# Kernel optimization log

Measured on AMD Instinct MI355X. Metric: run time of the kernel, lower is better.

Reference implementation:

```python
import jax, jax.numpy as jnp
import numpy as np

B, N, D_OBJ, D_Q, D_FUSED, D_BOX, D_ATT = 64, 36, 2048, 2048, 2048, 4, 512


def setup_inputs() -> dict:
    key = jax.random.key(0)
    ks = jax.random.split(key, 12)
    s = lambda d: 1.0 / np.sqrt(d)
    return {
        "question_embedding": jax.random.normal(ks[0], (B * N, D_Q), jnp.float32),
        "object_features_list": jax.random.normal(ks[1], (B, N, D_OBJ), jnp.float32),
        "bounding_boxes": jax.random.uniform(ks[2], (B, N, D_BOX), jnp.float32),
        "Wq": jax.random.normal(ks[3], (D_Q, D_FUSED), jnp.float32) * s(D_Q),
        "Wo": jax.random.normal(ks[4], (D_OBJ, D_FUSED), jnp.float32) * s(D_OBJ),
        "Wfa": jax.random.normal(ks[5], (D_FUSED, D_FUSED), jnp.float32) * s(D_FUSED),
        "Wfb": jax.random.normal(ks[6], (D_FUSED, D_FUSED), jnp.float32) * s(D_FUSED),
        "Wba": jax.random.normal(ks[7], (D_BOX, D_FUSED), jnp.float32) * s(D_BOX),
        "Wbb": jax.random.normal(ks[8], (D_BOX, D_FUSED), jnp.float32) * s(D_BOX),
        "W0": jax.random.normal(ks[9], (D_FUSED, D_ATT), jnp.float32) * s(D_FUSED),
        "b0": jnp.zeros((D_ATT,), jnp.float32),
        "W1": jax.random.normal(ks[10], (D_ATT, 1), jnp.float32) * s(D_ATT),
        "b1": jnp.zeros((1,), jnp.float32),
        "batch_size": B,
        "num_obj": N,
    }


def reference(question_embedding, object_features_list, bounding_boxes,
              Wq, Wo, Wfa, Wfb, Wba, Wbb, W0, b0, W1, b1,
              batch_size, num_obj):
    # fuse_object_features_with_questions: MLB fusion of question and objects
    obj_flat = object_features_list.reshape(batch_size * num_obj, -1)  # [BN, D]
    fused = (question_embedding @ Wq) * (obj_flat @ Wo)                # [BN, Df]
    fused = fused.reshape(batch_size, num_obj, -1)                     # [B, N, Df]

    # pairwise: project once, broadcast-multiply instead of materializing
    # expanded [B*N*N, D] operands (same math as expand+view+fusion).
    ra = fused @ Wfa                 # [B, N, Df]
    rb = fused @ Wfb                 # [B, N, Df]
    ba = bounding_boxes @ Wba        # [B, N, Df]
    bb = bounding_boxes @ Wbb        # [B, N, Df]
    # relations[b, i, j, :] = fusion_fused(f_i, f_j) + fusion_box(box_i, box_j)
    relations = ra[:, :, None, :] * rb[:, None, :, :] + ba[:, :, None, :] * bb[:, None, :, :]  # [B,N,N,Df]

    # compute_relation_attention: linear-tanh-linear, softmax over dim=2
    h = jnp.tanh(relations @ W0 + b0)          # [B, N, N, D_att]
    scores = h @ W1 + b1                       # [B, N, N, 1]
    att = jax.nn.softmax(scores, axis=2)[..., 0]  # [B, N, N]
    e_hat = jnp.sum(relations * att[..., None], axis=2)  # [B, N, Df]

    pairwise_res = fused + e_hat
    return object_features_list + pairwise_res
```

## Files before the change

kernel.cpp:

```cpp
#include <hip/hip_runtime.h>
#include <hip/hip_bf16.h>
#include <math.h>

constexpr int kB    = 64;
constexpr int kN    = 36;
constexpr int kBN   = kB * kN;
constexpr int kD    = 2048;
constexpr int kDatt = 512;
constexpr int kPairs = kN * kN;

using bf16x8 = __attribute__((ext_vector_type(8))) short;
using f32x4  = __attribute__((ext_vector_type(4))) float;

typedef unsigned int u32;
typedef __attribute__((address_space(3))) u32 lds_u32;
typedef const __attribute__((address_space(1))) u32 glb_u32;

__device__ inline unsigned short f2bf(float f) {
    union { float f; unsigned u; } v; v.f = f;
    unsigned r = v.u + 0x7FFFu + ((v.u >> 16) & 1u);
    return (unsigned short)(r >> 16);
}

__global__ __launch_bounds__(256)
void kcvt(const float* __restrict__ x, unsigned short* __restrict__ y, int n4)
{
    int i = blockIdx.x * 256 + threadIdx.x;
    if (i < n4) {
        float4 v = ((const float4*)x)[i];
        ushort4 o = {f2bf(v.x), f2bf(v.y), f2bf(v.z), f2bf(v.w)};
        ((ushort4*)y)[i] = o;
    }
}

__global__ __launch_bounds__(256)
void ktrp(const float* __restrict__ W, unsigned short* __restrict__ WT, int nt)
{
    __shared__ float T[64][65];
    const int k0 = blockIdx.x * 64;
    const int n0 = blockIdx.y * 64;
    const int c = threadIdx.x & 63, r0 = threadIdx.x >> 6;
    #pragma unroll
    for (int rr = 0; rr < 64; rr += 4)
        T[r0 + rr][c] = W[(size_t)(k0 + r0 + rr) * nt + n0 + c];
    __syncthreads();
    #pragma unroll
    for (int rr = 0; rr < 64; rr += 4)
        WT[(size_t)(n0 + r0 + rr) * kD + k0 + c] = f2bf(T[c][r0 + rr]);
}

__global__ __launch_bounds__(64)
void krepack_w0(const unsigned short* __restrict__ W0T, unsigned short* __restrict__ W0s)
{
    const int kb    = blockIdx.x;
    const int chunk = blockIdx.y;
    const int g     = threadIdx.x;
    const int row = chunk * 16 + (g & 7) + ((g >> 5) << 3);
    const int cg8 = ((g >> 3) & 3) * 8;
    const uint4 v = *(const uint4*)&W0T[(size_t)row * kD + kb * 32 + cg8];
    *(uint4*)&W0s[(size_t)kb * 16384 + chunk * 512 + g * 8] = v;
}

__global__ __launch_bounds__(256)
void kgbox(const float* __restrict__ Wba, const float* __restrict__ Wbb,
           const float* __restrict__ W0, float* __restrict__ Gpart)
{
    __shared__ float red[4][64][17];
    const int ct = blockIdx.x;
    const int kc = blockIdx.y;
    const int cl = threadIdx.x & 63;
    const int kq = threadIdx.x >> 6;
    const int c  = ct * 64 + cl;

    float acc[16];
    #pragma unroll
    for (int t = 0; t < 16; ++t) acc[t] = 0.f;

    const int kbase = kc * 128 + kq * 32;
    for (int kk = 0; kk < 32; ++kk) {
        int k = kbase + kk;
        float w0 = W0[(size_t)k * kDatt + c];
        float a0 = Wba[k], a1 = Wba[kD + k], a2 = Wba[2 * kD + k], a3 = Wba[3 * kD + k];
        float b0 = Wbb[k] * w0, b1 = Wbb[kD + k] * w0,
              b2 = Wbb[2 * kD + k] * w0, b3 = Wbb[3 * kD + k] * w0;
        acc[0]  = fmaf(a0, b0, acc[0]);  acc[1]  = fmaf(a0, b1, acc[1]);
        acc[2]  = fmaf(a0, b2, acc[2]);  acc[3]  = fmaf(a0, b3, acc[3]);
        acc[4]  = fmaf(a1, b0, acc[4]);  acc[5]  = fmaf(a1, b1, acc[5]);
        acc[6]  = fmaf(a1, b2, acc[6]);  acc[7]  = fmaf(a1, b3, acc[7]);
        acc[8]  = fmaf(a2, b0, acc[8]);  acc[9]  = fmaf(a2, b1, acc[9]);
        acc[10] = fmaf(a2, b2, acc[10]); acc[11] = fmaf(a2, b3, acc[11]);
        acc[12] = fmaf(a3, b0, acc[12]); acc[13] = fmaf(a3, b1, acc[13]);
        acc[14] = fmaf(a3, b2, acc[14]); acc[15] = fmaf(a3, b3, acc[15]);
    }
    #pragma unroll
    for (int t = 0; t < 16; ++t) red[kq][cl][t] = acc[t];
    __syncthreads();
    #pragma unroll
    for (int t = 0; t < 4; ++t) {
        int s = threadIdx.x + t * 256;
        int cc = s >> 4, uv = s & 15;
        float v = red[0][cc][uv] + red[1][cc][uv] + red[2][cc][uv] + red[3][cc][uv];
        Gpart[((size_t)kc * 16 + uv) * kDatt + ct * 64 + cc] = v;
    }
}

__global__ __launch_bounds__(64)
void krepack_g(const float* __restrict__ Gpart, unsigned short* __restrict__ W0s)
{
    const int chunk = blockIdx.x;
    const int g     = threadIdx.x;
    const int col = chunk * 16 + (g & 7) + ((g >> 5) << 3);
    const int kg  = (g >> 3) & 3;
    unsigned short o[8];
    #pragma unroll
    for (int e = 0; e < 8; ++e) {
        int kl = kg * 8 + e;
        if (kl < 16) {
            float s = 0.f;
            #pragma unroll
            for (int kc = 0; kc < 16; ++kc)
                s += Gpart[((size_t)kc * 16 + kl) * kDatt + col];
            o[e] = f2bf(s);
        } else o[e] = 0;
    }
    *(uint4*)&W0s[(size_t)64 * 16384 + chunk * 512 + g * 8] = *(uint4*)o;
}

__device__ inline void stage128(const unsigned short* __restrict__ g,
                                int grow0, int k0,
                                unsigned short* lds, int w, int lane)
{
    const int sr = lane >> 2, sc = (lane & 3) * 8;
    #pragma unroll
    for (int t = 0; t < 2; ++t) {
        int r = w * 32 + t * 16;
        const unsigned short* gp = g + (size_t)(grow0 + r + sr) * kD + k0 + sc;
        __builtin_amdgcn_global_load_lds((glb_u32*)gp, (lds_u32*)(lds + r * 32), 16, 0, 0);
    }
}
__device__ inline void stage64(const unsigned short* __restrict__ g,
                               int grow0, int k0,
                               unsigned short* lds, int w, int lane)
{
    const int sr = lane >> 2, sc = (lane & 3) * 8;
    int r = w * 16;
    const unsigned short* gp = g + (size_t)(grow0 + r + sr) * kD + k0 + sc;
    __builtin_amdgcn_global_load_lds((glb_u32*)gp, (lds_u32*)(lds + r * 32), 16, 0, 0);
}

__global__ __launch_bounds__(256, 2)
void k1_dual_mfma(const unsigned short* __restrict__ Qb,
                  const unsigned short* __restrict__ WqT,
                  const unsigned short* __restrict__ Ob,
                  const unsigned short* __restrict__ WoT,
                  unsigned short* __restrict__ fusedb)
{
    __shared__ __align__(16) unsigned short As1[128][32];
    __shared__ __align__(16) unsigned short As2[128][32];
    __shared__ __align__(16) unsigned short Bs1[64][32];
    __shared__ __align__(16) unsigned short Bs2[64][32];

    const int tid = threadIdx.x;
    const int lane = tid & 63;
    const int w = tid >> 6;
    const int wm = w >> 1, wn = w & 1;
    const int row0 = blockIdx.y * 128;
    const int col0 = blockIdx.x * 64;

    f32x4 acc1[4][2], acc2[4][2];
    #pragma unroll
    for (int mt = 0; mt < 4; ++mt)
        #pragma unroll
        for (int nt = 0; nt < 2; ++nt) { acc1[mt][nt] = (f32x4)(0.f); acc2[mt][nt] = (f32x4)(0.f); }

    const int fr = lane & 15, ko = (lane >> 4) * 8;

    for (int k0 = 0; k0 < kD; k0 += 32) {
        stage128(Qb,  row0, k0, &As1[0][0], w, lane);
        stage128(Ob,  row0, k0, &As2[0][0], w, lane);
        stage64 (WqT, col0, k0, &Bs1[0][0], w, lane);
        stage64 (WoT, col0, k0, &Bs2[0][0], w, lane);
        __syncthreads();

        bf16x8 a1[4], a2[4];
        #pragma unroll
        for (int mt = 0; mt < 4; ++mt) {
            a1[mt] = *(bf16x8*)&As1[wm * 64 + mt * 16 + fr][ko];
            a2[mt] = *(bf16x8*)&As2[wm * 64 + mt * 16 + fr][ko];
        }
        #pragma unroll
        for (int nt = 0; nt < 2; ++nt) {
            bf16x8 b1 = *(bf16x8*)&Bs1[wn * 32 + nt * 16 + fr][ko];
            bf16x8 b2 = *(bf16x8*)&Bs2[wn * 32 + nt * 16 + fr][ko];
            #pragma unroll
            for (int mt = 0; mt < 4; ++mt) {
                acc1[mt][nt] = __builtin_amdgcn_mfma_f32_16x16x32_bf16(a1[mt], b1, acc1[mt][nt], 0, 0, 0);
                acc2[mt][nt] = __builtin_amdgcn_mfma_f32_16x16x32_bf16(a2[mt], b2, acc2[mt][nt], 0, 0, 0);
            }
        }
        __syncthreads();
    }

    const int fq = lane >> 4;
    #pragma unroll
    for (int mt = 0; mt < 4; ++mt)
        #pragma unroll
        for (int nt = 0; nt < 2; ++nt) {
            int row = row0 + wm * 64 + mt * 16 + fq * 4;
            int col = col0 + wn * 32 + nt * 16 + fr;
            #pragma unroll
            for (int reg = 0; reg < 4; ++reg) {
                float v = acc1[mt][nt][reg] * acc2[mt][nt][reg];
                fusedb[(size_t)(row + reg) * kD + col] = f2bf(v);
            }
        }
}

__global__ __launch_bounds__(256, 2)
void k2_dual_mfma(const unsigned short* __restrict__ Fb,
                  const unsigned short* __restrict__ WfaT,
                  const unsigned short* __restrict__ WfbT,
                  float* __restrict__ ra, float* __restrict__ rb)
{
    __shared__ __align__(16) unsigned short As [128][32];
    __shared__ __align__(16) unsigned short Bs1[64][32];
    __shared__ __align__(16) unsigned short Bs2[64][32];

    const int tid = threadIdx.x;
    const int lane = tid & 63;
    const int w = tid >> 6;
    const int wm = w >> 1, wn = w & 1;
    const int row0 = blockIdx.y * 128;
    const int col0 = blockIdx.x * 64;

    f32x4 acc1[4][2], acc2[4][2];
    #pragma unroll
    for (int mt = 0; mt < 4; ++mt)
        #pragma unroll
        for (int nt = 0; nt < 2; ++nt) { acc1[mt][nt] = (f32x4)(0.f); acc2[mt][nt] = (f32x4)(0.f); }

    const int fr = lane & 15, ko = (lane >> 4) * 8;

    for (int k0 = 0; k0 < kD; k0 += 32) {
        stage128(Fb,   row0, k0, &As [0][0], w, lane);
        stage64 (WfaT, col0, k0, &Bs1[0][0], w, lane);
        stage64 (WfbT, col0, k0, &Bs2[0][0], w, lane);
        __syncthreads();

        bf16x8 a[4];
        #pragma unroll
        for (int mt = 0; mt < 4; ++mt)
            a[mt] = *(bf16x8*)&As[wm * 64 + mt * 16 + fr][ko];
        #pragma unroll
        for (int nt = 0; nt < 2; ++nt) {
            bf16x8 b1 = *(bf16x8*)&Bs1[wn * 32 + nt * 16 + fr][ko];
            bf16x8 b2 = *(bf16x8*)&Bs2[wn * 32 + nt * 16 + fr][ko];
            #pragma unroll
            for (int mt = 0; mt < 4; ++mt) {
                acc1[mt][nt] = __builtin_amdgcn_mfma_f32_16x16x32_bf16(a[mt], b1, acc1[mt][nt], 0, 0, 0);
                acc2[mt][nt] = __builtin_amdgcn_mfma_f32_16x16x32_bf16(a[mt], b2, acc2[mt][nt], 0, 0, 0);
            }
        }
        __syncthreads();
    }

    const int fq = lane >> 4;
    #pragma unroll
    for (int mt = 0; mt < 4; ++mt)
        #pragma unroll
        for (int nt = 0; nt < 2; ++nt) {
            int row = row0 + wm * 64 + mt * 16 + fq * 4;
            int col = col0 + wn * 32 + nt * 16 + fr;
            #pragma unroll
            for (int reg = 0; reg < 4; ++reg) {
                size_t o = (size_t)(row + reg) * kD + col;
                ra[o] = acc1[mt][nt][reg];
                rb[o] = acc2[mt][nt][reg];
            }
        }
}

__global__ __launch_bounds__(1024)
void k4_scores_mfma(const float* __restrict__ ra, const float* __restrict__ rb,
                    const float* __restrict__ box,
                    const unsigned short* __restrict__ W0s,
                    const float* __restrict__ b0, const float* __restrict__ W1,
                    float* __restrict__ scores)
{
    __shared__ __align__(16) unsigned short Bs[2][512 * 32];
    __shared__ __align__(16) unsigned short RelS[2][128][40];
    __shared__ __align__(16) float4 Stg4[2][378];
    __shared__ float scoreS[128];

    const int tid  = threadIdx.x;
    const int lane = tid & 63;
    const int w    = tid >> 6;
    const int wm   = w >> 3;
    const int wn   = w & 7;

    const int work = (blockIdx.x & 7) * 88 + (blockIdx.x >> 3);
    const int b    = work / 11;
    const int tile = work - b * 11;
    const int p0   = tile * 128;
    const int i0   = p0 / kN;

    const float* raB  = ra  + (size_t)b * kN * kD;
    const float* rbB  = rb  + (size_t)b * kN * kD;
    const float* boxB = box + (size_t)b * kN * 4;

    const bool hasStage = (tid < 336);
    const float* sptr;
    int sdst;
    {
        int s = hasStage ? tid : 335;
        int row = s >> 3, q = s & 7;
        int grow; const float* base;
        if (row < 6) {
            int il = (row < 5) ? row : 4;
            grow = i0 + il; if (grow > kN - 1) grow = kN - 1;
            base = raB;
        } else {
            grow = row - 6;
            base = rbB;
        }
        sptr = base + (size_t)grow * kD + q * 4;
        sdst = row * 9 + q;
    }

    int rowA, cgA, ilA, iA, jA;
    {
        rowA = tid >> 3; cgA = tid & 7;
        int p = p0 + rowA; if (p >= kPairs) p = kPairs - 1;
        iA  = p / kN;
        jA  = p - iA * kN;
        ilA = iA - i0;
    }

    const int fr = lane & 15, fq = lane >> 4;
    const int bco = ((fr & 7) << 3) + ((fr >> 3) << 8) + (fq << 6);

    f32x4 acc[4][4];
    #pragma unroll
    for (int mt = 0; mt < 4; ++mt)
        #pragma unroll
        for (int nt = 0; nt < 4; ++nt)
            acc[mt][nt] = (f32x4)(0.f);

    if (tid < 128) scoreS[tid] = 0.f;

    float4 sreg0;

    #define ISSUE_B(k0_, buf_)                                                   \
        _Pragma("unroll")                                                        \
        for (int t = 0; t < 2; ++t) {                                            \
            int chunk = w * 2 + t;                                               \
            const unsigned short* gp = W0s + (size_t)((k0_) >> 5) * 16384        \
                                       + chunk * 512 + lane * 8;                 \
            __builtin_amdgcn_global_load_lds((glb_u32*)gp,                       \
                (lds_u32*)&Bs[buf_][chunk * 512], 16, 0, 0);                     \
        }

    #define STAGE_LOAD(k0_) {                                                    \
            if (hasStage) sreg0 = *(const float4*)(sptr + (k0_));                \
        }

    #define STAGE_WRITE(buf_) {                                                  \
            if (hasStage) Stg4[buf_][sdst] = sreg0;                              \
        }

    #define REL_GEN(buf_) {                                                      \
            float4 va = Stg4[buf_][ilA * 9 + cgA];                               \
            float4 vr = Stg4[buf_][(6 + jA) * 9 + cgA];                          \
            ushort4 o;                                                           \
            o.x = f2bf(va.x * vr.x);                                             \
            o.y = f2bf(va.y * vr.y);                                             \
            o.z = f2bf(va.z * vr.z);                                             \
            o.w = f2bf(va.w * vr.w);                                             \
            *(ushort4*)&RelS[buf_][rowA][cgA * 4] = o;                           \
        }

    #define REL_GEN_BOX(buf_) {                                                  \
            ushort4 o = {0, 0, 0, 0};                                            \
            if (cgA < 4) {                                                       \
                float4 bi = *(const float4*)(boxB + iA * 4);                     \
                float4 bj = *(const float4*)(boxB + jA * 4);                     \
                float biu = (cgA == 0) ? bi.x : (cgA == 1) ? bi.y                \
                          : (cgA == 2) ? bi.z : bi.w;                            \
                o.x = f2bf(biu * bj.x);                                          \
                o.y = f2bf(biu * bj.y);                                          \
                o.z = f2bf(biu * bj.z);                                          \
                o.w = f2bf(biu * bj.w);                                          \
            }                                                                    \
            *(ushort4*)&RelS[buf_][rowA][cgA * 4] = o;                           \
        }

    STAGE_LOAD(0)
    STAGE_WRITE(0)
    STAGE_LOAD(32)
    __syncthreads();
    REL_GEN(0)
    STAGE_WRITE(1)
    ISSUE_B(0, 0)

    for (int k = 0; k <= 64; ++k) {
        const int cur = k & 1, nxt = cur ^ 1;
        __syncthreads();
        if (k < 62) STAGE_LOAD((k + 2) * 32)
        if (k < 64) ISSUE_B((k + 1) * 32, nxt)
        bf16x8 af[4];
        #pragma unroll
        for (int mt = 0; mt < 4; ++mt)
            af[mt] = *(bf16x8*)&RelS[cur][wm * 64 + mt * 16 + fr][fq * 8];
        if (k < 63) REL_GEN(nxt)
        else if (k == 63) REL_GEN_BOX(nxt)
        __builtin_amdgcn_s_setprio(1);
        #pragma unroll
        for (int nt = 0; nt < 4; ++nt) {
            bf16x8 bfv = *(bf16x8*)&Bs[cur][wn * 2048 + nt * 512 + bco];
            #pragma unroll
            for (int mt = 0; mt < 4; ++mt)
                acc[mt][nt] = __builtin_amdgcn_mfma_f32_16x16x32_bf16(af[mt], bfv, acc[mt][nt], 0, 0, 0);
        }
        __builtin_amdgcn_s_setprio(0);
        if (k < 62) STAGE_WRITE(cur)
    }

    float b0v[4], w1v[4];
    #pragma unroll
    for (int nt = 0; nt < 4; ++nt) {
        int col = wn * 64 + nt * 16 + fr;
        b0v[nt] = b0[col];
        w1v[nt] = W1[col];
    }
    #pragma unroll
    for (int mt = 0; mt < 4; ++mt) {
        #pragma unroll
        for (int reg = 0; reg < 4; ++reg) {
            float p = 0.f;
            #pragma unroll
            for (int nt = 0; nt < 4; ++nt)
                p += w1v[nt] * tanhf(acc[mt][nt][reg] + b0v[nt]);
            p += __shfl_xor(p, 1, 64);
            p += __shfl_xor(p, 2, 64);
            p += __shfl_xor(p, 4, 64);
            p += __shfl_xor(p, 8, 64);
            if (fr == 0)
                atomicAdd(&scoreS[wm * 64 + mt * 16 + fq * 4 + reg], p);
        }
    }
    __syncthreads();
    if (tid < 128 && p0 + tid < kPairs)
        scores[(size_t)b * kPairs + p0 + tid] = scoreS[tid];
}

__global__ __launch_bounds__(64)
void k5_softmax(const float* __restrict__ scores, const float* __restrict__ box,
                float* __restrict__ att, float* __restrict__ abox)
{
    const int bi = blockIdx.x;
    const int b  = bi / kN;
    const int tid = threadIdx.x;
    float s = (tid < kN) ? scores[(size_t)bi * kN + tid] : -1e30f;
    float m = s;
    #pragma unroll
    for (int off = 32; off >= 1; off >>= 1)
        m = fmaxf(m, __shfl_xor(m, off, 64));
    float e = (tid < kN) ? expf(s - m) : 0.f;
    float sum = e;
    #pragma unroll
    for (int off = 32; off >= 1; off >>= 1)
        sum += __shfl_xor(sum, off, 64);
    float a = e / sum;
    if (tid < kN) att[(size_t)bi * kN + tid] = a;

    float4 bx = {0.f, 0.f, 0.f, 0.f};
    if (tid < kN) bx = *(const float4*)(box + (size_t)(b * kN + tid) * 4);
    bx.x *= a; bx.y *= a; bx.z *= a; bx.w *= a;
    #pragma unroll
    for (int off = 32; off >= 1; off >>= 1) {
        bx.x += __shfl_xor(bx.x, off, 64);
        bx.y += __shfl_xor(bx.y, off, 64);
        bx.z += __shfl_xor(bx.z, off, 64);
        bx.w += __shfl_xor(bx.w, off, 64);
    }
    if (tid == 0) *(float4*)(abox + (size_t)bi * 4) = bx;
}

__global__ __launch_bounds__(256)
void k6_output(const float* __restrict__ obj, const unsigned short* __restrict__ fusedb,
               const float* __restrict__ ra, const float* __restrict__ rb,
               const float* __restrict__ att, const float* __restrict__ box,
               const float* __restrict__ abox,
               const float* __restrict__ Wba, const float* __restrict__ Wbb,
               float* __restrict__ out)
{
    __shared__ float attS[kN];
    const int bi = blockIdx.x;
    const int b = bi / kN;
    const int tid = threadIdx.x;
    if (tid < kN) attS[tid] = att[(size_t)bi * kN + tid];
    __syncthreads();
    const float4 bxi = *(const float4*)(box  + (size_t)bi * 4);
    const float4 axi = *(const float4*)(abox + (size_t)bi * 4);
    for (int d = tid; d < kD; d += 256) {
        float s1 = 0.f;
        #pragma unroll 4
        for (int j = 0; j < kN; ++j)
            s1 = fmaf(attS[j], rb[(size_t)(b * kN + j) * kD + d], s1);
        float bav = bxi.x * Wba[d] + bxi.y * Wba[kD + d]
                  + bxi.z * Wba[2 * kD + d] + bxi.w * Wba[3 * kD + d];
        float s2  = axi.x * Wbb[d] + axi.y * Wbb[kD + d]
                  + axi.z * Wbb[2 * kD + d] + axi.w * Wbb[3 * kD + d];
        size_t o = (size_t)bi * kD + d;
        float fv = __uint_as_float((u32)fusedb[o] << 16);
        out[o] = obj[o] + fv + ra[o] * s1 + bav * s2;
    }
}

extern "C" void kernel_launch(void* const* d_in, const int* in_sizes, int n_in,
                              void* d_out, int out_size, void* d_ws, size_t ws_size,
                              hipStream_t stream)
{
    const float* q   = (const float*)d_in[0];
    const float* obj = (const float*)d_in[1];
    const float* box = (const float*)d_in[2];
    const float* Wq  = (const float*)d_in[3];
    const float* Wo  = (const float*)d_in[4];
    const float* Wfa = (const float*)d_in[5];
    const float* Wfb = (const float*)d_in[6];
    const float* Wba = (const float*)d_in[7];
    const float* Wbb = (const float*)d_in[8];
    const float* W0  = (const float*)d_in[9];
    const float* b0v = (const float*)d_in[10];
    const float* W1  = (const float*)d_in[11];
    float* out = (float*)d_out;

    const size_t nBD = (size_t)kBN * kD;
    float* ws = (float*)d_ws;
    size_t off = 0;
    float* ra     = ws + off; off += nBD;
    float* rb     = ws + off; off += nBD;
    float* scores = ws + off; off += (size_t)kBN * kN;
    float* att    = ws + off; off += (size_t)kBN * kN;
    float* abox   = ws + off; off += (size_t)kBN * 4;
    float* Gpart  = ws + off; off += (size_t)16 * 16 * kDatt;

    unsigned short* us = (unsigned short*)(ws + off);
    size_t uoff = 0;
    unsigned short* W0T     = us + uoff; uoff += (size_t)kDatt * kD;
    unsigned short* W0s     = us + uoff; uoff += (size_t)65 * 16384;
    unsigned short* q_bf    = us + uoff; uoff += nBD;
    unsigned short* obj_bf  = us + uoff; uoff += nBD;
    unsigned short* fusedbf = us + uoff; uoff += nBD;
    unsigned short* WqT     = us + uoff; uoff += (size_t)kD * kD;
    unsigned short* WoT     = us + uoff; uoff += (size_t)kD * kD;
    unsigned short* WfaT = q_bf;
    unsigned short* WfbT = obj_bf;

    const int n4 = (int)(nBD / 4);
    kcvt<<<dim3((n4 + 255) / 256), 256, 0, stream>>>(q,   q_bf,   n4);
    kcvt<<<dim3((n4 + 255) / 256), 256, 0, stream>>>(obj, obj_bf, n4);
    ktrp<<<dim3(32, 32), 256, 0, stream>>>(Wq, WqT, kD);
    ktrp<<<dim3(32, 32), 256, 0, stream>>>(Wo, WoT, kD);
    ktrp<<<dim3(32, 8),  256, 0, stream>>>(W0, W0T, kDatt);
    krepack_w0<<<dim3(kD / 32, kDatt / 16), 64, 0, stream>>>(W0T, W0s);
    kgbox<<<dim3(8, 16), 256, 0, stream>>>(Wba, Wbb, W0, Gpart);
    krepack_g<<<dim3(32), 64, 0, stream>>>(Gpart, W0s);

    k1_dual_mfma<<<dim3(kD / 64, kBN / 128), 256, 0, stream>>>(q_bf, WqT, obj_bf, WoT, fusedbf);

    ktrp<<<dim3(32, 32), 256, 0, stream>>>(Wfa, WfaT, kD);
    ktrp<<<dim3(32, 32), 256, 0, stream>>>(Wfb, WfbT, kD);

    k2_dual_mfma<<<dim3(kD / 64, kBN / 128), 256, 0, stream>>>(fusedbf, WfaT, WfbT, ra, rb);

    k4_scores_mfma<<<dim3(kB * 11), 1024, 0, stream>>>(ra, rb, box, W0s, b0v, W1, scores);
    k5_softmax<<<kBN, 64, 0, stream>>>(scores, box, att, abox);
    k6_output<<<kBN, 256, 0, stream>>>(obj, fusedbf, ra, rb, att, box, abox, Wba, Wbb, out);
}
```

Measured before the change: 658.3 us.

## Split score kernel across two attention-column halves with atomic accumulation

The relation-attention score kernel now splits the 512 attention columns into two halves handled by separate 512-thread blocks, doubling the grid. Each block accumulates its partial score into a pre-zeroed scores buffer with global atomics, and a zeroing kernel is added before launch. The smaller blocks and halved B-tile shared memory are meant to improve occupancy and scheduling. In exchange, the relation products and staging loads are computed redundantly in both halves, and atomics make the summation order nondeterministic.

```diff
diff --git a/kernel.cpp b/kernel.cpp
--- a/kernel.cpp
+++ b/kernel.cpp
@@ -31,6 +31,13 @@
         ushort4 o = {f2bf(v.x), f2bf(v.y), f2bf(v.z), f2bf(v.w)};
         ((ushort4*)y)[i] = o;
     }
+}
+
+__global__ __launch_bounds__(256)
+void kzero(float* __restrict__ p, int n)
+{
+    int i = blockIdx.x * 256 + threadIdx.x;
+    if (i < n) p[i] = 0.f;
 }
 
 __global__ __launch_bounds__(256)
@@ -280,14 +287,14 @@
         }
 }
 
-__global__ __launch_bounds__(1024)
+__global__ __launch_bounds__(512, 4)
 void k4_scores_mfma(const float* __restrict__ ra, const float* __restrict__ rb,
                     const float* __restrict__ box,
                     const unsigned short* __restrict__ W0s,
                     const float* __restrict__ b0, const float* __restrict__ W1,
                     float* __restrict__ scores)
 {
-    __shared__ __align__(16) unsigned short Bs[2][512 * 32];
+    __shared__ __align__(16) unsigned short Bs[2][256 * 32];
     __shared__ __align__(16) unsigned short RelS[2][128][40];
     __shared__ __align__(16) float4 Stg4[2][378];
     __shared__ float scoreS[128];
@@ -295,12 +302,14 @@
     const int tid  = threadIdx.x;
     const int lane = tid & 63;
     const int w    = tid >> 6;
-    const int wm   = w >> 3;
-    const int wn   = w & 7;
-
-    const int work = (blockIdx.x & 7) * 88 + (blockIdx.x >> 3);
-    const int b    = work / 11;
-    const int tile = work - b * 11;
+    const int wm   = w >> 2;
+    const int wn   = w & 3;
+
+    const int work = (blockIdx.x & 7) * 176 + (blockIdx.x >> 3);
+    const int colb = work & 1;
+    const int wt   = work >> 1;
+    const int b    = wt / 11;
+    const int tile = wt - b * 11;
     const int p0   = tile * 128;
     const int i0   = p0 / kN;
 
@@ -327,13 +336,15 @@
         sdst = row * 9 + q;
     }
 
-    int rowA, cgA, ilA, iA, jA;
+    int rowA, cg2, iA, jA, sA, sR;
     {
-        rowA = tid >> 3; cgA = tid & 7;
+        rowA = tid >> 2; cg2 = tid & 3;
         int p = p0 + rowA; if (p >= kPairs) p = kPairs - 1;
-        iA  = p / kN;
-        jA  = p - iA * kN;
-        ilA = iA - i0;
+        iA = p / kN;
+        jA = p - iA * kN;
+        int ilA = iA - i0;
+        sA = ilA * 9 + cg2 * 2;
+        sR = (6 + jA) * 9 + cg2 * 2;
     }
 
     const int fr = lane & 15, fq = lane >> 4;
@@ -353,11 +364,11 @@
     #define ISSUE_B(k0_, buf_)                                                   \
         _Pragma("unroll")                                                        \
         for (int t = 0; t < 2; ++t) {                                            \
-            int chunk = w * 2 + t;                                               \
+            int ch = w * 2 + t;                                                  \
             const unsigned short* gp = W0s + (size_t)((k0_) >> 5) * 16384        \
-                                       + chunk * 512 + lane * 8;                 \
+                                       + (colb * 16 + ch) * 512 + lane * 8;      \
             __builtin_amdgcn_global_load_lds((glb_u32*)gp,                       \
-                (lds_u32*)&Bs[buf_][chunk * 512], 16, 0, 0);                     \
+                (lds_u32*)&Bs[buf_][ch * 512], 16, 0, 0);                        \
         }
 
     #define STAGE_LOAD(k0_) {                                                    \
@@ -369,29 +380,28 @@
         }
 
     #define REL_GEN(buf_) {                                                      \
-            float4 va = Stg4[buf_][ilA * 9 + cgA];                               \
-            float4 vr = Stg4[buf_][(6 + jA) * 9 + cgA];                          \
-            ushort4 o;                                                           \
-            o.x = f2bf(va.x * vr.x);                                             \
-            o.y = f2bf(va.y * vr.y);                                             \
-            o.z = f2bf(va.z * vr.z);                                             \
-            o.w = f2bf(va.w * vr.w);                                             \
-            *(ushort4*)&RelS[buf_][rowA][cgA * 4] = o;                           \
+            float4 va0 = Stg4[buf_][sA],     va1 = Stg4[buf_][sA + 1];           \
+            float4 vr0 = Stg4[buf_][sR],     vr1 = Stg4[buf_][sR + 1];           \
+            unsigned short o[8];                                                 \
+            o[0] = f2bf(va0.x * vr0.x); o[1] = f2bf(va0.y * vr0.y);              \
+            o[2] = f2bf(va0.z * vr0.z); o[3] = f2bf(va0.w * vr0.w);              \
+            o[4] = f2bf(va1.x * vr1.x); o[5] = f2bf(va1.y * vr1.y);              \
+            o[6] = f2bf(va1.z * vr1.z); o[7] = f2bf(va1.w * vr1.w);              \
+            *(bf16x8*)&RelS[buf_][rowA][cg2 * 8] = *(bf16x8*)o;                  \
         }
 
     #define REL_GEN_BOX(buf_) {                                                  \
-            ushort4 o = {0, 0, 0, 0};                                            \
-            if (cgA < 4) {                                                       \
-                float4 bi = *(const float4*)(boxB + iA * 4);                     \
+            unsigned short o[8] = {0, 0, 0, 0, 0, 0, 0, 0};                      \
+            if (cg2 < 2) {                                                       \
                 float4 bj = *(const float4*)(boxB + jA * 4);                     \
-                float biu = (cgA == 0) ? bi.x : (cgA == 1) ? bi.y                \
-                          : (cgA == 2) ? bi.z : bi.w;                            \
-                o.x = f2bf(biu * bj.x);                                          \
-                o.y = f2bf(biu * bj.y);                                          \
-                o.z = f2bf(biu * bj.z);                                          \
-                o.w = f2bf(biu * bj.w);                                          \
+                float biu0 = boxB[iA * 4 + cg2 * 2];                             \
+                float biu1 = boxB[iA * 4 + cg2 * 2 + 1];                         \
+                o[0] = f2bf(biu0 * bj.x); o[1] = f2bf(biu0 * bj.y);              \
+                o[2] = f2bf(biu0 * bj.z); o[3] = f2bf(biu0 * bj.w);              \
+                o[4] = f2bf(biu1 * bj.x); o[5] = f2bf(biu1 * bj.y);              \
+                o[6] = f2bf(biu1 * bj.z); o[7] = f2bf(biu1 * bj.w);              \
             }                                                                    \
-            *(ushort4*)&RelS[buf_][rowA][cgA * 4] = o;                           \
+            *(bf16x8*)&RelS[buf_][rowA][cg2 * 8] = *(bf16x8*)o;                  \
         }
 
     STAGE_LOAD(0)
@@ -428,7 +438,7 @@
     float b0v[4], w1v[4];
     #pragma unroll
     for (int nt = 0; nt < 4; ++nt) {
-        int col = wn * 64 + nt * 16 + fr;
+        int col = colb * 256 + wn * 64 + nt * 16 + fr;
         b0v[nt] = b0[col];
         w1v[nt] = W1[col];
     }
@@ -450,7 +460,7 @@
     }
     __syncthreads();
     if (tid < 128 && p0 + tid < kPairs)
-        scores[(size_t)b * kPairs + p0 + tid] = scoreS[tid];
+        atomicAdd(&scores[(size_t)b * kPairs + p0 + tid], scoreS[tid]);
 }
 
 __global__ __launch_bounds__(64)
@@ -566,6 +576,7 @@
     krepack_w0<<<dim3(kD / 32, kDatt / 16), 64, 0, stream>>>(W0T, W0s);
     kgbox<<<dim3(8, 16), 256, 0, stream>>>(Wba, Wbb, W0, Gpart);
     krepack_g<<<dim3(32), 64, 0, stream>>>(Gpart, W0s);
+    kzero<<<dim3((kBN * kN + 255) / 256), 256, 0, stream>>>(scores, kBN * kN);
 
     k1_dual_mfma<<<dim3(kD / 64, kBN / 128), 256, 0, stream>>>(q_bf, WqT, obj_bf, WoT, fusedbf);
 
@@ -574,7 +585,7 @@
 
     k2_dual_mfma<<<dim3(kD / 64, kBN / 128), 256, 0, stream>>>(fusedbf, WfaT, WfbT, ra, rb);
 
-    k4_scores_mfma<<<dim3(kB * 11), 1024, 0, stream>>>(ra, rb, box, W0s, b0v, W1, scores);
+    k4_scores_mfma<<<dim3(kB * 11 * 2), 512, 0, stream>>>(ra, rb, box, W0s, b0v, W1, scores);
     k5_softmax<<<kBN, 64, 0, stream>>>(scores, box, att, abox);
     k6_output<<<kBN, 256, 0, stream>>>(obj, fusedbf, ra, rb, att, box, abox, Wba, Wbb, out);
 }
```

Measured after the change: 645.7 us. Within noise of the previous version (-1.9%).
